# Performance work log

Hardware: AMD Instinct MI355X
Metric: run time of the kernel (lower is better)

The kernel has to match this reference:

```python
import jax, jax.numpy as jnp
import numpy as np
from jax import lax

S = 64        # num_sam_segments
B = 2
HIMG = 336    # full-res SAM segmap / painted map
HP = 24       # DINO patch grid (336/14)
CD = 768      # DINO feature channels
CM = 3072     # concatenated backbone channels (4 layers * 768)
RH = 48       # readout spatial size ceil(336/7)
HID = 128     # SPADE hidden_mlp_channels
EPS = 1e-12


def conv2d(x, w, b=None, pad=0):
    out = lax.conv_general_dilated(x, w, (1, 1), [(pad, pad), (pad, pad)],
                                   dimension_numbers=("NCHW", "OIHW", "NCHW"))
    if b is not None:
        out = out + b[None, :, None, None]
    return out


def paint_semantic_map(f_sem, segmap):
    # f_sem: (B, C, Hp, Wp) float; segmap: (B, H, W) int
    Bn, C, Hp, Wp = f_sem.shape
    H, W = segmap.shape[1:]
    # torch F.interpolate mode='nearest' downsample: src_idx = floor(dst_idx * in/out)
    iy = (jnp.arange(Hp) * H) // Hp
    ix = (jnp.arange(Wp) * W) // Wp
    seg_p = segmap[:, iy][:, :, ix]                      # (B, Hp, Wp)
    ids = jnp.clip(seg_p, 0, S - 1).reshape(Bn, -1)      # (B, Np)
    ids_off = (ids + jnp.arange(Bn)[:, None] * S).reshape(-1)
    flat = f_sem.transpose(0, 2, 3, 1).reshape(Bn * Hp * Wp, C)
    sums = jax.ops.segment_sum(flat, ids_off, num_segments=Bn * S)
    cnt = jax.ops.segment_sum(jnp.ones((Bn * Hp * Wp, 1), flat.dtype), ids_off,
                              num_segments=Bn * S)
    means = jnp.where(cnt > 0, sums / jnp.maximum(cnt, 1.0), 0.0).reshape(Bn, S, C)
    pix = jnp.clip(segmap, 0, S - 1)                     # (B, H, W)
    painted = means[jnp.arange(Bn)[:, None, None], pix]  # (B, H, W, C) gather
    return painted.transpose(0, 3, 1, 2)                 # (B, C, H, W)


def spade_ln(x, painted, ws, bs, wg, bg, wb, bb):
    # layer_norm over (C,H,W) per sample, no affine
    mean = jnp.mean(x, axis=(1, 2, 3), keepdims=True)
    var = jnp.mean((x - mean) ** 2, axis=(1, 2, 3), keepdims=True)
    xn = (x - mean) * lax.rsqrt(var + EPS)
    sem = jax.image.resize(painted, (x.shape[0], painted.shape[1], x.shape[2], x.shape[3]),
                           method="bilinear")
    h = jax.nn.relu(conv2d(sem, ws, bs, pad=1))
    gamma = conv2d(h, wg, bg, pad=1)
    beta = conv2d(h, wb, bb, pad=1)
    return xn * (1.0 + gamma) + beta


def setup_inputs() -> dict:
    key = jax.random.key(0)
    ks = jax.random.split(key, 16)
    n = lambda k, sh: jax.random.normal(k, sh, jnp.float32) * 0.02
    inp = {
        "x_main": jax.random.normal(ks[0], (B, CM, RH, RH), jnp.float32),
        "f_sem": jax.random.normal(ks[1], (B, CD, HP, HP), jnp.float32),
        "segmap": jax.random.randint(ks[2], (B, HIMG, HIMG), 0, S, jnp.int32),
    }
    i = 3
    for li, nf in enumerate([CM, 8, 16]):
        inp[f"ws{li}"] = n(ks[i], (HID, CD, 3, 3)); inp[f"bs{li}"] = jnp.zeros((HID,), jnp.float32)
        inp[f"wg{li}"] = n(ks[i + 1], (nf, HID, 3, 3)); inp[f"bg{li}"] = jnp.zeros((nf,), jnp.float32)
        inp[f"wb{li}"] = n(ks[i + 2], (nf, HID, 3, 3)); inp[f"bb{li}"] = jnp.zeros((nf,), jnp.float32)
        i += 3
    inp["w0"] = n(ks[12], (8, CM, 1, 1)); inp["bias0"] = jnp.zeros((8,), jnp.float32)
    inp["w1"] = n(ks[13], (16, 8, 1, 1)); inp["bias1"] = jnp.zeros((16,), jnp.float32)
    inp["w2"] = n(ks[14], (1, 16, 1, 1)); inp["bias2"] = jnp.zeros((1,), jnp.float32)
    return inp


def reference(x_main, f_sem, segmap,
              ws0, bs0, wg0, bg0, wb0, bb0,
              ws1, bs1, wg1, bg1, wb1, bb1,
              ws2, bs2, wg2, bg2, wb2, bb2,
              w0, bias0, w1, bias1, w2, bias2):
    painted = paint_semantic_map(f_sem, segmap)
    h = spade_ln(x_main, painted, ws0, bs0, wg0, bg0, wb0, bb0)
    h = jax.nn.softplus(conv2d(h, w0) + bias0[None, :, None, None])
    h = spade_ln(h, painted, ws1, bs1, wg1, bg1, wb1, bb1)
    h = jax.nn.softplus(conv2d(h, w1) + bias1[None, :, None, None])
    h = spade_ln(h, painted, ws2, bs2, wg2, bg2, wb2, bb2)
    h = jax.nn.softplus(conv2d(h, w2) + bias2[None, :, None, None])
    return h  # (B, 1, RH, RH)
```

## Files before the change

kernel.cpp:

```cpp
#include <hip/hip_runtime.h>
#include <hip/hip_bf16.h>

typedef __hip_bfloat16 bf16;
typedef __bf16 v8bf __attribute__((ext_vector_type(8)));
typedef float v4f __attribute__((ext_vector_type(4)));

#define PB 2304
#define PTOT 4608

__device__ __forceinline__ float b2f(bf16 x){ return __bfloat162float(x); }
__device__ __forceinline__ bf16 f2b(float x){ return __float2bfloat16(x); }
__device__ __forceinline__ float softplus_f(float x){
  return fmaxf(x, 0.f) + log1pf(expf(-fabsf(x)));
}
__device__ __forceinline__ float LD(const void* src, size_t i, int fl){
  return fl ? ((const float*)src)[i] : b2f(((const bf16*)src)[i]);
}

__device__ __forceinline__ void gload_lds16(const void* g, void* l){
  __builtin_amdgcn_global_load_lds(
      (const __attribute__((address_space(1))) void*)g,
      (__attribute__((address_space(3))) void*)l, 16, 0, 0);
}

__global__ __launch_bounds__(256) void k_sniff(const unsigned* __restrict__ x, int* __restrict__ flag){
  int t = threadIdx.x;
  int cnt = 0;
  for (int i = t; i < 4096; i += 256){
    unsigned e = (x[i] >> 8) & 0x7F;
    if (e >= 0x38 && e <= 0x42) cnt++;
  }
  for (int off = 32; off; off >>= 1) cnt += __shfl_down(cnt, off, 64);
  __shared__ int sc[4];
  if ((t & 63) == 0) sc[t >> 6] = cnt;
  __syncthreads();
  if (t == 0) *flag = (sc[0]+sc[1]+sc[2]+sc[3] < 2048) ? 1 : 0;
}

__global__ void k_zero(float* __restrict__ p, int n){
  int i = blockIdx.x*256 + threadIdx.x;
  if (i < n) p[i] = 0.f;
}

__global__ __launch_bounds__(256) void k_cvt_small(
    const void* s4, const void* s10, const void* s16, const void* s6, const void* s8,
    const void* s12, const void* s14, const void* s18, const void* s20,
    const void* s21, const void* s22, const void* s23, const void* s24,
    const void* s25, const void* s26,
    float* __restrict__ dst, const int* __restrict__ flag){
  int i = blockIdx.x*256 + threadIdx.x;
  if (i >= 31321) return;
  int fl = *flag;
  const void* src; size_t off;
  if      (i < 128)   { src = s4;  off = i; }
  else if (i < 256)   { src = s10; off = i - 128; }
  else if (i < 384)   { src = s16; off = i - 256; }
  else if (i < 3456)  { src = s6;  off = i - 384; }
  else if (i < 6528)  { src = s8;  off = i - 3456; }
  else if (i < 6536)  { src = s12; off = i - 6528; }
  else if (i < 6544)  { src = s14; off = i - 6536; }
  else if (i < 6560)  { src = s18; off = i - 6544; }
  else if (i < 6576)  { src = s20; off = i - 6560; }
  else if (i < 31152) { src = s21; off = i - 6576; }
  else if (i < 31160) { src = s22; off = i - 31152; }
  else if (i < 31288) { src = s23; off = i - 31160; }
  else if (i < 31304) { src = s24; off = i - 31288; }
  else if (i < 31320) { src = s25; off = i - 31304; }
  else                { src = s26; off = i - 31320; }
  dst[i] = LD(src, off, fl);
}

__global__ __launch_bounds__(256) void k_bcol(const float* __restrict__ SMALLF, float* __restrict__ BCOL){
  int t = threadIdx.x;
  const float* BG1 = SMALLF + 6528; const float* BB1 = SMALLF + 6536;
  const float* BG2 = SMALLF + 6544; const float* BB2 = SMALLF + 6560;
  const float* BB0 = SMALLF + 3456; const float* W0  = SMALLF + 6576;
  if (t < 8)       BCOL[t] = BG1[t];
  else if (t < 16) BCOL[t] = BB1[t-8];
  else if (t < 32) BCOL[t] = BG2[t-16];
  else if (t < 48) BCOL[t] = BB2[t-32];
  else if (t < 64) BCOL[t] = 0.f;
  float part[8] = {0,0,0,0,0,0,0,0};
  for (int c = t; c < 3072; c += 256){
    float bb = BB0[c];
    #pragma unroll
    for (int oc = 0; oc < 8; oc++) part[oc] += bb*W0[oc*3072 + c];
  }
  __shared__ float red[4][8];
  int wv = t >> 6, lane = t & 63;
  #pragma unroll
  for (int oc = 0; oc < 8; oc++){
    float v = part[oc];
    for (int off = 32; off; off >>= 1) v += __shfl_down(v, off, 64);
    if (lane == 0) red[wv][oc] = v;
  }
  __syncthreads();
  if (t < 8) BCOL[48 + t] = red[0][t] + red[1][t] + red[2][t] + red[3][t];
}

__global__ __launch_bounds__(256) void k_mzero(float* __restrict__ MB){
  int i = blockIdx.x*256 + threadIdx.x;
  if (i < 9216) MB[i] = 0.f;
}

__global__ __launch_bounds__(256) void k_mbeta(const void* __restrict__ wb0, const int* __restrict__ flag,
                                               const float* __restrict__ w0f, float* __restrict__ MB){
  int jb = blockIdx.x, nb = blockIdx.y, t = threadIdx.x;
  int fl = *flag;
  int jl = t & 127, nh = t >> 7;
  int j = jb*128 + jl;
  int src = jl*9 + jb;
  float acc[8] = {0,0,0,0,0,0,0,0};
  int n0 = nb*128 + nh*64;
  for (int i = 0; i < 64; i++){
    int n = n0 + i;
    float wv = LD(wb0, (size_t)n*1152 + src, fl);
    #pragma unroll
    for (int oc = 0; oc < 8; oc++) acc[oc] += wv*w0f[oc*3072 + n];
  }
  #pragma unroll
  for (int oc = 0; oc < 8; oc++) atomicAdd(&MB[oc*1152 + j], acc[oc]);
}

__global__ __launch_bounds__(256) void k_wsm(const float* __restrict__ MB, bf16* __restrict__ WSMALL){
  int i = blockIdx.x*256 + threadIdx.x;
  if (i >= 9216) return;
  float v = MB[i];
  bf16 hi = f2b(v);
  WSMALL[48*1152 + i] = hi;
  WSMALL[56*1152 + i] = f2b(v - b2f(hi));
}

template<int ICW>
__global__ __launch_bounds__(256) void k_permW(const void* __restrict__ src, bf16* __restrict__ dst,
                                               int total, const int* __restrict__ flag){
  int idx = blockIdx.x*256 + threadIdx.x;
  if (idx >= total) return;
  int oc = idx / (9*ICW);
  int rr = idx % (9*ICW);
  int dyx = rr / ICW, ic = rr % ICW;
  size_t si = (size_t)(oc*ICW + ic)*9 + dyx;
  dst[idx] = f2b(LD(src, si, *flag));
}

__global__ __launch_bounds__(256) void k_seg_means(const void* __restrict__ f_sem, const int* __restrict__ flag,
                                                   const int* __restrict__ segmap,
                                                   float* __restrict__ means){
  int s = blockIdx.x, b = blockIdx.y, t = threadIdx.x;
  int fl = *flag;
  __shared__ int sid[576];
  for (int i = t; i < 576; i += 256){
    int y = i / 24, x = i % 24;
    int v = segmap[b*336*336 + (y*14)*336 + x*14];
    sid[i] = min(max(v, 0), 63);
  }
  __syncthreads();
  float a0=0.f, a1=0.f, a2=0.f; int cnt = 0;
  for (int i = 0; i < 576; i++){
    if (sid[i] == s){
      cnt++;
      a0 += LD(f_sem, (size_t)(b*768 + t      )*576 + i, fl);
      a1 += LD(f_sem, (size_t)(b*768 + t + 256)*576 + i, fl);
      a2 += LD(f_sem, (size_t)(b*768 + t + 512)*576 + i, fl);
    }
  }
  float inv = cnt > 0 ? 1.f/(float)cnt : 0.f;
  float* o = means + (size_t)(b*64 + s)*768;
  o[t] = a0*inv; o[t+256] = a1*inv; o[t+512] = a2*inv;
}

__global__ __launch_bounds__(256) void k_tt(const void* __restrict__ ws0, const void* __restrict__ ws1,
    const void* __restrict__ ws2, const int* __restrict__ flag,
    const float* __restrict__ means, bf16* __restrict__ WTT){
  int bx = blockIdx.x;
  int dyx = bx / 24, ocb = bx % 24;
  int b = blockIdx.y, t = threadIdx.x;
  int fl = *flag;
  int ocg0 = ocb*16;
  const void* wsrc; int ocl0 = ocg0;
  if (ocl0 < 128) wsrc = ws0;
  else if (ocl0 < 256){ wsrc = ws1; ocl0 -= 128; }
  else { wsrc = ws2; ocl0 -= 256; }
  __shared__ float wl[16][768];
  for (int ol = 0; ol < 16; ol++)
    for (int ic = t; ic < 768; ic += 256)
      wl[ol][ic] = LD(wsrc, (size_t)(ocl0 + ol)*6912 + (size_t)ic*9 + dyx, fl);
  __syncthreads();
  int s = t & 63, og = t >> 6;
  const float* mr = means + ((size_t)b*64 + s)*768;
  float acc[4] = {0.f, 0.f, 0.f, 0.f};
  for (int ic = 0; ic < 768; ic += 4){
    float4 m = *reinterpret_cast<const float4*>(mr + ic);
    #pragma unroll
    for (int k = 0; k < 4; k++){
      const float* w = &wl[og + k*4][ic];
      acc[k] += m.x*w[0] + m.y*w[1] + m.z*w[2] + m.w*w[3];
    }
  }
  #pragma unroll
  for (int k = 0; k < 4; k++){
    bf16 h = f2b(acc[k]);
    size_t base = ((size_t)(b*384 + ocg0 + og + k*4))*1152 + (size_t)dyx*128 + s;
    WTT[base] = h;
    WTT[base + 64] = h;
  }
}

__global__ __launch_bounds__(192) void k_A(const int* __restrict__ segmap, bf16* __restrict__ AHL){
  int blk = blockIdx.x;
  int b = blk / PB, rem = blk % PB, yo = rem / 48, xo = rem % 48;
  __shared__ float accs[64];
  int t = threadIdx.x;
  if (t < 64) accs[t] = 0.f;
  __syncthreads();
  if (t < 169){
    int ty = t / 13, tx = t % 13;
    int jy = 7*yo - 3 + ty, jx = 7*xo - 3 + tx;
    if (jy >= 0 && jy < 336 && jx >= 0 && jx < 336){
      int wy = 7 - abs(ty - 6), wx = 7 - abs(tx - 6);
      int sv = segmap[b*336*336 + jy*336 + jx];
      sv = min(max(sv, 0), 63);
      atomicAdd(&accs[sv], (float)(wy*wx));
    }
  }
  int sumy = 0, sumx = 0;
  for (int k = 0; k < 13; k++){
    int jy = 7*yo - 3 + k; if (jy >= 0 && jy < 336) sumy += 7 - abs(k - 6);
    int jx = 7*xo - 3 + k; if (jx >= 0 && jx < 336) sumx += 7 - abs(k - 6);
  }
  __syncthreads();
  if (t < 64){
    float v = accs[t] / (float)(sumy*sumx);
    bf16 hi = f2b(v);
    AHL[(size_t)blk*128 + t] = hi;
    AHL[(size_t)blk*128 + 64 + t] = f2b(v - b2f(hi));
  }
}

__global__ __launch_bounds__(256) void k_ln_partial(const void* __restrict__ x, const int* __restrict__ flag,
                                                    float2* __restrict__ part){
  int b = blockIdx.y, blk = blockIdx.x, t = threadIdx.x;
  int fl = *flag;
  size_t base = (size_t)b*7077888 + (size_t)blk*55296;
  float s = 0.f, sq = 0.f;
  for (int i = 0; i < 216; i++){
    float v = LD(x, base + t + i*256, fl);
    s += v; sq += v*v;
  }
  for (int off = 32; off; off >>= 1){ s += __shfl_down(s, off, 64); sq += __shfl_down(sq, off, 64); }
  __shared__ float ls[4], lq[4];
  int w = t >> 6, lane = t & 63;
  if (lane == 0){ ls[w] = s; lq[w] = sq; }
  __syncthreads();
  if (t == 0) part[b*128 + blk] = make_float2(ls[0]+ls[1]+ls[2]+ls[3], lq[0]+lq[1]+lq[2]+lq[3]);
}

__global__ void k_ln_final(const float2* __restrict__ part, float* __restrict__ stats){
  int b = blockIdx.x, t = threadIdx.x;
  float2 v = part[b*128 + t];
  float s = v.x, sq = v.y;
  for (int off = 32; off; off >>= 1){ s += __shfl_down(s, off, 64); sq += __shfl_down(sq, off, 64); }
  __shared__ float ls[2], lq[2];
  if ((t & 63) == 0){ ls[t>>6] = s; lq[t>>6] = sq; }
  __syncthreads();
  if (t == 0){
    s = ls[0]+ls[1]; sq = lq[0]+lq[1];
    const float N = 7077888.f;
    float mean = s/N; float var = sq/N - mean*mean; var = fmaxf(var, 0.f);
    stats[b*2] = mean; stats[b*2+1] = rsqrtf(var + 1e-12f);
  }
}

__global__ __launch_bounds__(256) void k_ln_small(const float* __restrict__ z, int cnt, float* __restrict__ stats){
  int b = blockIdx.x, t = threadIdx.x;
  const float* p = z + (size_t)b*cnt;
  float s = 0.f, sq = 0.f;
  for (int i = t; i < cnt; i += 256){ float v = p[i]; s += v; sq += v*v; }
  for (int off = 32; off; off >>= 1){ s += __shfl_down(s, off, 64); sq += __shfl_down(sq, off, 64); }
  __shared__ float ls[4], lq[4];
  int w = t >> 6, lane = t & 63;
  if (lane == 0){ ls[w] = s; lq[w] = sq; }
  __syncthreads();
  if (t == 0){
    s = ls[0]+ls[1]+ls[2]+ls[3]; sq = lq[0]+lq[1]+lq[2]+lq[3];
    float mean = s/(float)cnt; float var = sq/(float)cnt - mean*mean; var = fmaxf(var, 0.f);
    stats[b*2] = mean; stats[b*2+1] = rsqrtf(var + 1e-12f);
  }
}

template<bool RELU, typename OT>
__global__ __launch_bounds__(256) void k_gemm(
    const bf16* __restrict__ Asrc, int AS, int acol, int ICW,
    const bf16* __restrict__ W, int K, size_t wbstride,
    const float* __restrict__ bp0, const float* __restrict__ bp1, const float* __restrict__ bp2, int seg,
    OT* __restrict__ out, int N, int ncb, int ldo, const bf16* __restrict__ zpad)
{
  __shared__ __align__(16) bf16 Al[64][64];
  __shared__ __align__(16) bf16 Bl[64][64];
  int t = threadIdx.x;
  int m0 = blockIdx.x*64, n0 = blockIdx.y*64;
  int wv = t >> 6, lane = t & 63;
  int lr8 = lane >> 3, sseg = (lane & 7) ^ lr8;
  int b = m0 >= PB ? 1 : 0;

  int ya[2], xa[2]; bool bv[2]; const bf16* wb[2];
  #pragma unroll
  for (int i = 0; i < 2; i++){
    int sp = (m0 - b*PB) + wv*16 + i*8 + lr8;
    ya[i] = sp / 48; xa[i] = sp % 48;
    int nrow = ncb + n0 + wv*16 + i*8 + lr8;
    bv[i] = nrow < N;
    wb[i] = W + (size_t)b*wbstride + (size_t)nrow*K + sseg*8;
  }

  int wm = (wv >> 1)*32, wn = (wv & 1)*32;
  int lrow = lane & 15, quad = lane >> 4;
  int sx = lrow & 7;
  int o0 = ((quad    ) ^ sx)*8;
  int o1 = ((quad + 4) ^ sx)*8;

  v4f acc00 = {0,0,0,0}, acc01 = {0,0,0,0}, acc10 = {0,0,0,0}, acc11 = {0,0,0,0};

  int dyx = 0, ic0 = 0;
  int ktn = K / 64;
  for (int kt = 0; kt < ktn; kt++){
    int dy = dyx/3 - 1, dx = dyx%3 - 1;
    #pragma unroll
    for (int i = 0; i < 2; i++){
      int ys = ya[i] + dy, xs = xa[i] + dx;
      const bf16* ga = (ys >= 0 && ys < 48 && xs >= 0 && xs < 48)
        ? Asrc + (size_t)(b*PB + ys*48 + xs)*AS + acol + ic0 + sseg*8 : zpad;
      gload_lds16(ga, &Al[wv*16 + i*8][0]);
      const bf16* gb = bv[i] ? wb[i] + kt*64 : zpad;
      gload_lds16(gb, &Bl[wv*16 + i*8][0]);
    }
    asm volatile("s_waitcnt vmcnt(0)" ::: "memory");
    __syncthreads();
    v8bf a00 = *reinterpret_cast<const v8bf*>(&Al[wm      + lrow][o0]);
    v8bf a10 = *reinterpret_cast<const v8bf*>(&Al[wm + 16 + lrow][o0]);
    v8bf a01 = *reinterpret_cast<const v8bf*>(&Al[wm      + lrow][o1]);
    v8bf a11 = *reinterpret_cast<const v8bf*>(&Al[wm + 16 + lrow][o1]);
    v8bf b00 = *reinterpret_cast<const v8bf*>(&Bl[wn      + lrow][o0]);
    v8bf b10 = *reinterpret_cast<const v8bf*>(&Bl[wn + 16 + lrow][o0]);
    v8bf b01 = *reinterpret_cast<const v8bf*>(&Bl[wn      + lrow][o1]);
    v8bf b11 = *reinterpret_cast<const v8bf*>(&Bl[wn + 16 + lrow][o1]);
    acc00 = __builtin_amdgcn_mfma_f32_16x16x32_bf16(a00, b00, acc00, 0, 0, 0);
    acc00 = __builtin_amdgcn_mfma_f32_16x16x32_bf16(a01, b01, acc00, 0, 0, 0);
    acc01 = __builtin_amdgcn_mfma_f32_16x16x32_bf16(a00, b10, acc01, 0, 0, 0);
    acc01 = __builtin_amdgcn_mfma_f32_16x16x32_bf16(a01, b11, acc01, 0, 0, 0);
    acc10 = __builtin_amdgcn_mfma_f32_16x16x32_bf16(a10, b00, acc10, 0, 0, 0);
    acc10 = __builtin_amdgcn_mfma_f32_16x16x32_bf16(a11, b01, acc10, 0, 0, 0);
    acc11 = __builtin_amdgcn_mfma_f32_16x16x32_bf16(a10, b10, acc11, 0, 0, 0);
    acc11 = __builtin_amdgcn_mfma_f32_16x16x32_bf16(a11, b11, acc11, 0, 0, 0);
    __syncthreads();
    ic0 += 64; if (ic0 == ICW){ ic0 = 0; dyx++; }
  }

  auto store_tile = [&](v4f a, int mi, int ni){
    int gcol = ncb + n0 + wn + ni*16 + lrow;
    if (gcol >= N) return;
    int sel = gcol / seg; sel = sel > 2 ? 2 : sel;
    const float* bp = sel == 0 ? bp0 : (sel == 1 ? bp1 : bp2);
    float bias = bp[gcol - sel*seg];
    int rowb = m0 + wm + mi*16 + quad*4;
    #pragma unroll
    for (int rg = 0; rg < 4; rg++){
      float v = a[rg] + bias;
      if (RELU) v = fmaxf(v, 0.f);
      if constexpr (sizeof(OT) == 2) out[(size_t)(rowb+rg)*ldo + (gcol - ncb)] = f2b(v);
      else                           out[(size_t)(rowb+rg)*ldo + (gcol - ncb)] = (OT)v;
    }
  };
  store_tile(acc00, 0, 0); store_tile(acc01, 0, 1);
  store_tile(acc10, 1, 0); store_tile(acc11, 1, 1);
}

__global__ __launch_bounds__(256) void k_gfuse(
    const bf16* __restrict__ HS, const bf16* __restrict__ WG0, const float* __restrict__ BG0,
    const void* __restrict__ x, const int* __restrict__ flag, const float* __restrict__ stats,
    const float* __restrict__ w0f, float* __restrict__ z0, const bf16* __restrict__ zpad)
{
  __shared__ __align__(16) char lds_raw[38912];
  bf16 (*Al)[64]  = (bf16(*)[64])lds_raw;
  bf16 (*Bl)[64]  = (bf16(*)[64])(lds_raw + 16384);
  float (*xl)[132] = (float(*)[132])lds_raw;
  float (*w0l)[128] = (float(*)[128])(lds_raw + 33792);
  float* bg0l = (float*)(lds_raw + 33792 + 4096);

  int t = threadIdx.x;
  int m0 = blockIdx.x*128, n0 = blockIdx.y*128;
  int b = m0 >= PB ? 1 : 0;
  int fl = *flag;

  int wv = t >> 6, lane = t & 63;
  int lr8 = lane >> 3, sseg = (lane & 7) ^ lr8;
  int spbase = m0 - b*PB;

  int ya[4], xa[4];
  #pragma unroll
  for (int i = 0; i < 4; i++){
    int sp = spbase + wv*32 + i*8 + lr8;
    ya[i] = sp / 48; xa[i] = sp % 48;
  }
  const bf16* wgb = WG0 + (size_t)(n0 + wv*32 + lr8)*1152 + sseg*8;

  int wm = wv*32, lrow = lane & 15, quad = lane >> 4;
  int sx = lrow & 7;

  v4f acc[2][8];
  #pragma unroll
  for (int mi = 0; mi < 2; mi++)
    #pragma unroll
    for (int ni = 0; ni < 8; ni++) acc[mi][ni] = (v4f){0,0,0,0};

  for (int kt = 0; kt < 18; kt++){
    int dyx = kt >> 1, icr = (kt & 1) << 6;
    int dy = dyx/3 - 1, dx = dyx%3 - 1;
    #pragma unroll
    for (int i = 0; i < 4; i++){
      int ys = ya[i] + dy, xs = xa[i] + dx;
      const bf16* ga = (ys >= 0 && ys < 48 && xs >= 0 && xs < 48)
        ? HS + (size_t)(b*PB + ys*48 + xs)*384 + icr + sseg*8 : zpad;
      gload_lds16(ga, &Al[wv*32 + i*8][0]);
      gload_lds16(wgb + (size_t)(i*8)*1152 + dyx*128 + icr, &Bl[wv*32 + i*8][0]);
    }
    asm volatile("s_waitcnt vmcnt(0)" ::: "memory");
    __syncthreads();
    #pragma unroll
    for (int kh = 0; kh < 2; kh++){
      int oa = ((kh*4 + quad) ^ sx)*8;
      v8bf a0 = *reinterpret_cast<const v8bf*>(&Al[wm      + lrow][oa]);
      v8bf a1 = *reinterpret_cast<const v8bf*>(&Al[wm + 16 + lrow][oa]);
      #pragma unroll
      for (int ni = 0; ni < 8; ni++){
        v8bf bn = *reinterpret_cast<const v8bf*>(&Bl[ni*16 + lrow][oa]);
        acc[0][ni] = __builtin_amdgcn_mfma_f32_16x16x32_bf16(a0, bn, acc[0][ni], 0, 0, 0);
        acc[1][ni] = __builtin_amdgcn_mfma_f32_16x16x32_bf16(a1, bn, acc[1][ni], 0, 0, 0);
      }
    }
    __syncthreads();
  }

  for (int i = t; i < 1024; i += 256) w0l[i >> 7][i & 127] = w0f[(size_t)(i >> 7)*3072 + n0 + (i & 127)];
  if (t < 128) bg0l[t] = BG0[n0 + t];

  float mean = stats[b*2], rstd = stats[b*2+1];
  float s[2][4][8];
  #pragma unroll
  for (int mi = 0; mi < 2; mi++)
    #pragma unroll
    for (int rg = 0; rg < 4; rg++)
      #pragma unroll
      for (int oc = 0; oc < 8; oc++) s[mi][rg][oc] = 0.f;

  for (int h = 0; h < 2; h++){
    if (h) __syncthreads();
    if (fl){
      const float* xp = (const float*)x + ((size_t)(b*3072 + n0 + h*64))*2304 + spbase;
      #pragma unroll
      for (int it = 0; it < 8; it++){
        int idx = it*256 + t;
        int row = idx >> 5, c4 = (idx & 31)*4;
        float4 v = *reinterpret_cast<const float4*>(xp + (size_t)row*2304 + c4);
        *reinterpret_cast<float4*>(&xl[row][c4]) = v;
      }
    } else {
      const bf16* xp = (const bf16*)x + ((size_t)(b*3072 + n0 + h*64))*2304 + spbase;
      #pragma unroll
      for (int it = 0; it < 4; it++){
        int idx = it*256 + t;
        int row = idx >> 4, c8 = (idx & 15)*8;
        v8bf v = *reinterpret_cast<const v8bf*>(xp + (size_t)row*2304 + c8);
        float4 f0, f1;
        f0.x = (float)v[0]; f0.y = (float)v[1]; f0.z = (float)v[2]; f0.w = (float)v[3];
        f1.x = (float)v[4]; f1.y = (float)v[5]; f1.z = (float)v[6]; f1.w = (float)v[7];
        *reinterpret_cast<float4*>(&xl[row][c8])     = f0;
        *reinterpret_cast<float4*>(&xl[row][c8 + 4]) = f1;
      }
    }
    __syncthreads();
    #pragma unroll
    for (int mi = 0; mi < 2; mi++){
      int pl = wm + mi*16 + quad*4;
      #pragma unroll
      for (int nis = 0; nis < 4; nis++){
        int ni = h*4 + nis;
        int c_half = nis*16 + lrow;
        int c_blk = h*64 + c_half;
        float bg = bg0l[c_blk];
        float w0v[8];
        #pragma unroll
        for (int oc = 0; oc < 8; oc++) w0v[oc] = w0l[oc][c_blk];
        #pragma unroll
        for (int rg = 0; rg < 4; rg++){
          float gv = acc[mi][ni][rg] + bg;
          float xn = (xl[c_half][pl + rg] - mean)*rstd;
          float tv = xn*(1.f + gv);
          #pragma unroll
          for (int oc = 0; oc < 8; oc++) s[mi][rg][oc] += tv*w0v[oc];
        }
      }
    }
  }

  #pragma unroll
  for (int mi = 0; mi < 2; mi++){
    #pragma unroll
    for (int rg = 0; rg < 4; rg++)
      #pragma unroll
      for (int oc = 0; oc < 8; oc++){
        float v = s[mi][rg][oc];
        v += __shfl_xor(v, 1, 64);
        v += __shfl_xor(v, 2, 64);
        v += __shfl_xor(v, 4, 64);
        v += __shfl_xor(v, 8, 64);
        s[mi][rg][oc] = v;
      }
    if (lrow == 0){
      int p = m0 + wm + mi*16 + quad*4;
      #pragma unroll
      for (int rg = 0; rg < 4; rg++)
        #pragma unroll
        for (int oc = 0; oc < 8; oc++)
          atomicAdd(&z0[(size_t)(p + rg)*8 + oc], s[mi][rg][oc]);
    }
  }
}

__global__ __launch_bounds__(256) void k_z0init(const float* __restrict__ b0f, const float* __restrict__ GBS,
                                                float* __restrict__ z0){
  int i = blockIdx.x*256 + threadIdx.x;
  if (i >= 36864) return;
  int p = i >> 3, oc = i & 7;
  z0[i] = b0f[oc] + GBS[(size_t)p*64 + 48 + oc] + GBS[(size_t)p*64 + 56 + oc];
}

__global__ __launch_bounds__(256) void k_sp(float* z, int n){
  int i = blockIdx.x*256 + threadIdx.x;
  if (i < n) z[i] = softplus_f(z[i]);
}

__global__ __launch_bounds__(256) void k_F1(const float* __restrict__ z0, const float* __restrict__ GBS,
    const float* __restrict__ stats, const float* __restrict__ w1f, const float* __restrict__ b1f,
    float* __restrict__ z1){
  int p = blockIdx.x*256 + threadIdx.x;
  if (p >= PTOT) return;
  int b = p / PB;
  float mean = stats[b*2], rstd = stats[b*2+1];
  const float* zr = z0 + (size_t)p*8;
  const float* gr = GBS + (size_t)p*64;
  float yv[8];
  #pragma unroll
  for (int c = 0; c < 8; c++) yv[c] = (zr[c] - mean)*rstd*(1.f + gr[c]) + gr[8 + c];
  #pragma unroll
  for (int oc = 0; oc < 16; oc++){
    float s = b1f[oc];
    #pragma unroll
    for (int c = 0; c < 8; c++) s += yv[c]*w1f[oc*8 + c];
    z1[(size_t)p*16 + oc] = softplus_f(s);
  }
}

__global__ __launch_bounds__(256) void k_F2(const float* __restrict__ z1, const float* __restrict__ GBS,
    const float* __restrict__ stats, const float* __restrict__ w2f, const float* __restrict__ b2f,
    void* __restrict__ outp, const int* __restrict__ flag){
  int p = blockIdx.x*256 + threadIdx.x;
  if (p >= PTOT) return;
  int b = p / PB;
  float mean = stats[b*2], rstd = stats[b*2+1];
  const float* zr = z1 + (size_t)p*16;
  const float* gr = GBS + (size_t)p*64 + 16;
  float s = b2f[0];
  #pragma unroll
  for (int c = 0; c < 16; c++){
    float yv = (zr[c] - mean)*rstd*(1.f + gr[c]) + gr[16 + c];
    s += yv*w2f[c];
  }
  float r = softplus_f(s);
  if (*flag) ((float*)outp)[p] = r;
  else       ((bf16*)outp)[p] = f2b(r);
}

extern "C" void kernel_launch(void* const* d_in, const int* in_sizes, int n_in,
                              void* d_out, int out_size, void* d_ws, size_t ws_size,
                              hipStream_t stream){
  const void* x_main = d_in[0];
  const void* f_sem  = d_in[1];
  const int*  segmap = (const int*)d_in[2];

  char* ws = (char*)d_ws;
  size_t o = 0;
  auto alloc = [&](size_t bytes){ size_t r = o; o = (o + bytes + 255) & ~(size_t)255; return r; };
  float* MEANS = (float*)(ws + alloc(98304u*4));
  bf16*  AHL   = (bf16*) (ws + alloc(589824u*2));
  bf16*  WTT   = (bf16*) (ws + alloc(884736u*2));
  bf16*  WG0   = (bf16*) (ws + alloc(3538944u*2));
  bf16*  WSMALL= (bf16*) (ws + alloc(73728u*2));
  bf16*  HS    = (bf16*) (ws + alloc(1769472u*2));
  float* GBS   = (float*)(ws + alloc(294912u*4));
  float* Z0    = (float*)(ws + alloc(36864u*4));
  float* Z1    = (float*)(ws + alloc(73728u*4));
  float2* LNP  = (float2*)(ws + alloc(256u*8));
  float* STATS = (float*)(ws + alloc(16u*4));
  int*   FLAG  = (int*)  (ws + alloc(64u));
  float* SMALLF= (float*)(ws + alloc(31321u*4));
  float* MB    = (float*)(ws + alloc(9216u*4));
  float* BCOL  = (float*)(ws + alloc(64u*4));
  bf16*  ZPAD  = (bf16*) (ws + alloc(512u));

  float *BS0=SMALLF+0, *BS1=SMALLF+128, *BS2=SMALLF+256;
  float *BG0=SMALLF+384;
  float *W0=SMALLF+6576, *B0=SMALLF+31152;
  float *W1=SMALLF+31160, *B1=SMALLF+31288;
  float *W2=SMALLF+31304, *B2=SMALLF+31320;

  k_sniff<<<1, 256, 0, stream>>>((const unsigned*)x_main, FLAG);
  k_zero<<<1, 256, 0, stream>>>((float*)ZPAD, 128);
  k_cvt_small<<<123, 256, 0, stream>>>(d_in[4], d_in[10], d_in[16], d_in[6], d_in[8],
      d_in[12], d_in[14], d_in[18], d_in[20], d_in[21], d_in[22], d_in[23], d_in[24],
      d_in[25], d_in[26], SMALLF, FLAG);
  k_bcol<<<1, 256, 0, stream>>>(SMALLF, BCOL);
  k_mzero<<<36, 256, 0, stream>>>(MB);
  k_mbeta<<<dim3(9,24), 256, 0, stream>>>(d_in[7], FLAG, W0, MB);
  k_wsm<<<36, 256, 0, stream>>>(MB, WSMALL);

  k_permW<128><<<dim3((3538944+255)/256),256, 0, stream>>>(d_in[5],  WG0,            3538944, FLAG);
  k_permW<128><<<dim3((9216+255)/256),   256, 0, stream>>>(d_in[11], WSMALL,           9216, FLAG);
  k_permW<128><<<dim3((9216+255)/256),   256, 0, stream>>>(d_in[13], WSMALL + 8*1152,  9216, FLAG);
  k_permW<128><<<dim3((18432+255)/256),  256, 0, stream>>>(d_in[17], WSMALL + 16*1152, 18432, FLAG);
  k_permW<128><<<dim3((18432+255)/256),  256, 0, stream>>>(d_in[19], WSMALL + 32*1152, 18432, FLAG);

  k_ln_partial<<<dim3(128,2), 256, 0, stream>>>(x_main, FLAG, LNP);
  k_ln_final<<<2, 128, 0, stream>>>(LNP, STATS);
  k_seg_means<<<dim3(64,2), 256, 0, stream>>>(f_sem, FLAG, segmap, MEANS);
  k_tt<<<dim3(216,2), 256, 0, stream>>>(d_in[3], d_in[9], d_in[15], FLAG, MEANS, WTT);
  k_A<<<PTOT, 192, 0, stream>>>(segmap, AHL);

  k_gemm<true, bf16><<<dim3(72,6), 256, 0, stream>>>(AHL, 128, 0, 128, WTT, 1152, (size_t)384*1152,
      BS0, BS1, BS2, 128, HS, 384, 0, 384, ZPAD);
  k_gemm<false, float><<<dim3(72,1), 256, 0, stream>>>(HS, 384, 128, 128, WSMALL, 1152, 0,
      BCOL, BCOL, BCOL, 9999, GBS, 16, 0, 64, ZPAD);
  k_gemm<false, float><<<dim3(72,1), 256, 0, stream>>>(HS, 384, 256, 128, WSMALL + 16*1152, 1152, 0,
      BCOL+16, BCOL+16, BCOL+16, 9999, GBS+16, 32, 0, 64, ZPAD);
  k_gemm<false, float><<<dim3(72,1), 256, 0, stream>>>(HS, 384, 0, 128, WSMALL + 48*1152, 1152, 0,
      BCOL+48, BCOL+48, BCOL+48, 9999, GBS+48, 16, 0, 64, ZPAD);

  k_z0init<<<144, 256, 0, stream>>>(B0, GBS, Z0);
  k_gfuse<<<dim3(36,24), 256, 0, stream>>>(HS, WG0, BG0, x_main, FLAG, STATS, W0, Z0, ZPAD);
  k_sp<<<144, 256, 0, stream>>>(Z0, 36864);

  k_ln_small<<<2, 256, 0, stream>>>(Z0, 18432, STATS + 4);
  k_F1<<<18, 256, 0, stream>>>(Z0, GBS, STATS + 4, W1, B1, Z1);
  k_ln_small<<<2, 256, 0, stream>>>(Z1, 36864, STATS + 8);
  k_F2<<<18, 256, 0, stream>>>(Z1, GBS, STATS + 8, W2, B2, d_out, FLAG);
}
```

Baseline: 634.5 us.

## Halve gfuse N-tile for occupancy and fold small launches into fewer kernels

The main fused gamma-conv kernel drops its N tile from 128 to 64 channels, doubling the grid to 36x48. This shrinks the accumulator and output registers and allows a 4-blocks-per-CU launch bound, at the cost of reloading the A tile twice as often and doing more atomics on z0. Several tiny launches are merged: ZPAD zeroing goes into sniff, MB zeroing into cvt_small, the three small GEMMs into one grid, and softplus into the layernorm stats pass. The merges target launch overhead.

Result: faster. 621.7 us (-2.0%).

```diff
diff --git a/kernel.cpp b/kernel.cpp
--- a/kernel.cpp
+++ b/kernel.cpp
@@ -23,8 +23,10 @@
       (__attribute__((address_space(3))) void*)l, 16, 0, 0);
 }
 
-__global__ __launch_bounds__(256) void k_sniff(const unsigned* __restrict__ x, int* __restrict__ flag){
+__global__ __launch_bounds__(256) void k_sniff(const unsigned* __restrict__ x, int* __restrict__ flag,
+                                               float* __restrict__ zp){
   int t = threadIdx.x;
+  if (t < 128) zp[t] = 0.f;
   int cnt = 0;
   for (int i = t; i < 4096; i += 256){
     unsigned e = (x[i] >> 8) & 0x7F;
@@ -35,11 +37,6 @@
   if ((t & 63) == 0) sc[t >> 6] = cnt;
   __syncthreads();
   if (t == 0) *flag = (sc[0]+sc[1]+sc[2]+sc[3] < 2048) ? 1 : 0;
-}
-
-__global__ void k_zero(float* __restrict__ p, int n){
-  int i = blockIdx.x*256 + threadIdx.x;
-  if (i < n) p[i] = 0.f;
 }
 
 __global__ __launch_bounds__(256) void k_cvt_small(
@@ -47,9 +44,10 @@
     const void* s12, const void* s14, const void* s18, const void* s20,
     const void* s21, const void* s22, const void* s23, const void* s24,
     const void* s25, const void* s26,
-    float* __restrict__ dst, const int* __restrict__ flag){
+    float* __restrict__ dst, const int* __restrict__ flag, float* __restrict__ MB){
   int i = blockIdx.x*256 + threadIdx.x;
-  if (i >= 31321) return;
+  if (i >= 40537) return;
+  if (i >= 31321){ MB[i - 31321] = 0.f; return; }
   int fl = *flag;
   const void* src; size_t off;
   if      (i < 128)   { src = s4;  off = i; }
@@ -98,11 +96,6 @@
   if (t < 8) BCOL[48 + t] = red[0][t] + red[1][t] + red[2][t] + red[3][t];
 }
 
-__global__ __launch_bounds__(256) void k_mzero(float* __restrict__ MB){
-  int i = blockIdx.x*256 + threadIdx.x;
-  if (i < 9216) MB[i] = 0.f;
-}
-
 __global__ __launch_bounds__(256) void k_mbeta(const void* __restrict__ wb0, const int* __restrict__ flag,
                                                const float* __restrict__ w0f, float* __restrict__ MB){
   int jb = blockIdx.x, nb = blockIdx.y, t = threadIdx.x;
@@ -271,6 +264,27 @@
   }
 }
 
+__global__ __launch_bounds__(256) void k_spln(float* __restrict__ z, int cnt, float* __restrict__ stats){
+  int b = blockIdx.x, t = threadIdx.x;
+  float* p = z + (size_t)b*cnt;
+  float s = 0.f, sq = 0.f;
+  for (int i = t; i < cnt; i += 256){
+    float v = softplus_f(p[i]);
+    p[i] = v;
+    s += v; sq += v*v;
+  }
+  for (int off = 32; off; off >>= 1){ s += __shfl_down(s, off, 64); sq += __shfl_down(sq, off, 64); }
+  __shared__ float ls[4], lq[4];
+  int w = t >> 6, lane = t & 63;
+  if (lane == 0){ ls[w] = s; lq[w] = sq; }
+  __syncthreads();
+  if (t == 0){
+    s = ls[0]+ls[1]+ls[2]+ls[3]; sq = lq[0]+lq[1]+lq[2]+lq[3];
+    float mean = s/(float)cnt; float var = sq/(float)cnt - mean*mean; var = fmaxf(var, 0.f);
+    stats[b*2] = mean; stats[b*2+1] = rsqrtf(var + 1e-12f);
+  }
+}
+
 __global__ __launch_bounds__(256) void k_ln_small(const float* __restrict__ z, int cnt, float* __restrict__ stats){
   int b = blockIdx.x, t = threadIdx.x;
   const float* p = z + (size_t)b*cnt;
@@ -289,16 +303,14 @@
 }
 
 template<bool RELU, typename OT>
-__global__ __launch_bounds__(256) void k_gemm(
+__device__ __forceinline__ void gemm_body(
     const bf16* __restrict__ Asrc, int AS, int acol, int ICW,
     const bf16* __restrict__ W, int K, size_t wbstride,
     const float* __restrict__ bp0, const float* __restrict__ bp1, const float* __restrict__ bp2, int seg,
-    OT* __restrict__ out, int N, int ncb, int ldo, const bf16* __restrict__ zpad)
+    OT* __restrict__ out, int N, int ncb, int ldo, const bf16* __restrict__ zpad,
+    int m0, int n0, bf16 (*Al)[64], bf16 (*Bl)[64])
 {
-  __shared__ __align__(16) bf16 Al[64][64];
-  __shared__ __align__(16) bf16 Bl[64][64];
   int t = threadIdx.x;
-  int m0 = blockIdx.x*64, n0 = blockIdx.y*64;
   int wv = t >> 6, lane = t & 63;
   int lr8 = lane >> 3, sseg = (lane & 7) ^ lr8;
   int b = m0 >= PB ? 1 : 0;
@@ -375,20 +387,49 @@
   store_tile(acc10, 1, 0); store_tile(acc11, 1, 1);
 }
 
-__global__ __launch_bounds__(256) void k_gfuse(
+template<bool RELU, typename OT>
+__global__ __launch_bounds__(256) void k_gemm(
+    const bf16* __restrict__ Asrc, int AS, int acol, int ICW,
+    const bf16* __restrict__ W, int K, size_t wbstride,
+    const float* __restrict__ bp0, const float* __restrict__ bp1, const float* __restrict__ bp2, int seg,
+    OT* __restrict__ out, int N, int ncb, int ldo, const bf16* __restrict__ zpad)
+{
+  __shared__ __align__(16) bf16 Al[64][64];
+  __shared__ __align__(16) bf16 Bl[64][64];
+  gemm_body<RELU, OT>(Asrc, AS, acol, ICW, W, K, wbstride, bp0, bp1, bp2, seg,
+                      out, N, ncb, ldo, zpad, blockIdx.x*64, blockIdx.y*64, Al, Bl);
+}
+
+__global__ __launch_bounds__(256) void k_gsmall(
+    const bf16* __restrict__ HS, const bf16* __restrict__ WSMALL, const float* __restrict__ BCOL,
+    float* __restrict__ GBS, const bf16* __restrict__ zpad)
+{
+  __shared__ __align__(16) bf16 Al[64][64];
+  __shared__ __align__(16) bf16 Bl[64][64];
+  int y = blockIdx.y;
+  int acol = y == 0 ? 128 : (y == 1 ? 256 : 0);
+  const bf16* W = WSMALL + (y == 0 ? 0 : (y == 1 ? 16*1152 : 48*1152));
+  const float* bp = BCOL + (y == 0 ? 0 : (y == 1 ? 16 : 48));
+  float* out = GBS + (y == 0 ? 0 : (y == 1 ? 16 : 48));
+  int N = y == 1 ? 32 : 16;
+  gemm_body<false, float>(HS, 384, acol, 128, W, 1152, 0, bp, bp, bp, 9999,
+                          out, N, 0, 64, zpad, blockIdx.x*64, 0, Al, Bl);
+}
+
+__global__ __launch_bounds__(256, 4) void k_gfuse(
     const bf16* __restrict__ HS, const bf16* __restrict__ WG0, const float* __restrict__ BG0,
     const void* __restrict__ x, const int* __restrict__ flag, const float* __restrict__ stats,
     const float* __restrict__ w0f, float* __restrict__ z0, const bf16* __restrict__ zpad)
 {
-  __shared__ __align__(16) char lds_raw[38912];
+  __shared__ __align__(16) char lds_raw[36096];
   bf16 (*Al)[64]  = (bf16(*)[64])lds_raw;
   bf16 (*Bl)[64]  = (bf16(*)[64])(lds_raw + 16384);
   float (*xl)[132] = (float(*)[132])lds_raw;
-  float (*w0l)[128] = (float(*)[128])(lds_raw + 33792);
-  float* bg0l = (float*)(lds_raw + 33792 + 4096);
+  float (*w0l)[64] = (float(*)[64])(lds_raw + 33792);
+  float* bg0l = (float*)(lds_raw + 35840);
 
   int t = threadIdx.x;
-  int m0 = blockIdx.x*128, n0 = blockIdx.y*128;
+  int m0 = blockIdx.x*128, n0 = blockIdx.y*64;
   int b = m0 >= PB ? 1 : 0;
   int fl = *flag;
 
@@ -402,16 +443,16 @@
     int sp = spbase + wv*32 + i*8 + lr8;
     ya[i] = sp / 48; xa[i] = sp % 48;
   }
-  const bf16* wgb = WG0 + (size_t)(n0 + wv*32 + lr8)*1152 + sseg*8;
+  const bf16* wgb = WG0 + (size_t)(n0 + wv*16 + lr8)*1152 + sseg*8;
 
   int wm = wv*32, lrow = lane & 15, quad = lane >> 4;
   int sx = lrow & 7;
 
-  v4f acc[2][8];
+  v4f acc[2][4];
   #pragma unroll
   for (int mi = 0; mi < 2; mi++)
     #pragma unroll
-    for (int ni = 0; ni < 8; ni++) acc[mi][ni] = (v4f){0,0,0,0};
+    for (int ni = 0; ni < 4; ni++) acc[mi][ni] = (v4f){0,0,0,0};
 
   for (int kt = 0; kt < 18; kt++){
     int dyx = kt >> 1, icr = (kt & 1) << 6;
@@ -422,8 +463,10 @@
       const bf16* ga = (ys >= 0 && ys < 48 && xs >= 0 && xs < 48)
         ? HS + (size_t)(b*PB + ys*48 + xs)*384 + icr + sseg*8 : zpad;
       gload_lds16(ga, &Al[wv*32 + i*8][0]);
-      gload_lds16(wgb + (size_t)(i*8)*1152 + dyx*128 + icr, &Bl[wv*32 + i*8][0]);
-    }
+    }
+    #pragma unroll
+    for (int i = 0; i < 2; i++)
+      gload_lds16(wgb + (size_t)(i*8)*1152 + dyx*128 + icr, &Bl[wv*16 + i*8][0]);
     asm volatile("s_waitcnt vmcnt(0)" ::: "memory");
     __syncthreads();
     #pragma unroll
@@ -432,7 +475,7 @@
       v8bf a0 = *reinterpret_cast<const v8bf*>(&Al[wm      + lrow][oa]);
       v8bf a1 = *reinterpret_cast<const v8bf*>(&Al[wm + 16 + lrow][oa]);
       #pragma unroll
-      for (int ni = 0; ni < 8; ni++){
+      for (int ni = 0; ni < 4; ni++){
         v8bf bn = *reinterpret_cast<const v8bf*>(&Bl[ni*16 + lrow][oa]);
         acc[0][ni] = __builtin_amdgcn_mfma_f32_16x16x32_bf16(a0, bn, acc[0][ni], 0, 0, 0);
         acc[1][ni] = __builtin_amdgcn_mfma_f32_16x16x32_bf16(a1, bn, acc[1][ni], 0, 0, 0);
@@ -441,88 +484,85 @@
     __syncthreads();
   }
 
-  for (int i = t; i < 1024; i += 256) w0l[i >> 7][i & 127] = w0f[(size_t)(i >> 7)*3072 + n0 + (i & 127)];
-  if (t < 128) bg0l[t] = BG0[n0 + t];
+  for (int i = t; i < 512; i += 256) w0l[i >> 6][i & 63] = w0f[(size_t)(i >> 6)*3072 + n0 + (i & 63)];
+  if (t < 64) bg0l[t] = BG0[n0 + t];
+
+  if (fl){
+    const float* xp = (const float*)x + ((size_t)(b*3072 + n0))*2304 + spbase;
+    #pragma unroll
+    for (int it = 0; it < 8; it++){
+      int idx = it*256 + t;
+      int row = idx >> 5, c4 = (idx & 31)*4;
+      float4 v = *reinterpret_cast<const float4*>(xp + (size_t)row*2304 + c4);
+      *reinterpret_cast<float4*>(&xl[row][c4]) = v;
+    }
+  } else {
+    const bf16* xp = (const bf16*)x + ((size_t)(b*3072 + n0))*2304 + spbase;
+    #pragma unroll
+    for (int it = 0; it < 4; it++){
+      int idx = it*256 + t;
+      int row = idx >> 4, c8 = (idx & 15)*8;
+      v8bf v = *reinterpret_cast<const v8bf*>(xp + (size_t)row*2304 + c8);
+      float4 f0, f1;
+      f0.x = (float)v[0]; f0.y = (float)v[1]; f0.z = (float)v[2]; f0.w = (float)v[3];
+      f1.x = (float)v[4]; f1.y = (float)v[5]; f1.z = (float)v[6]; f1.w = (float)v[7];
+      *reinterpret_cast<float4*>(&xl[row][c8])     = f0;
+      *reinterpret_cast<float4*>(&xl[row][c8 + 4]) = f1;
+    }
+  }
+  __syncthreads();
 
   float mean = stats[b*2], rstd = stats[b*2+1];
-  float s[2][4][8];
-  #pragma unroll
-  for (int mi = 0; mi < 2; mi++)
-    #pragma unroll
-    for (int rg = 0; rg < 4; rg++)
+
+  for (int og2 = 0; og2 < 2; og2++){
+    float s[2][4][4];
+    #pragma unroll
+    for (int mi = 0; mi < 2; mi++)
       #pragma unroll
-      for (int oc = 0; oc < 8; oc++) s[mi][rg][oc] = 0.f;
-
-  for (int h = 0; h < 2; h++){
-    if (h) __syncthreads();
-    if (fl){
-      const float* xp = (const float*)x + ((size_t)(b*3072 + n0 + h*64))*2304 + spbase;
-      #pragma unroll
-      for (int it = 0; it < 8; it++){
-        int idx = it*256 + t;
-        int row = idx >> 5, c4 = (idx & 31)*4;
-        float4 v = *reinterpret_cast<const float4*>(xp + (size_t)row*2304 + c4);
-        *reinterpret_cast<float4*>(&xl[row][c4]) = v;
-      }
-    } else {
-      const bf16* xp = (const bf16*)x + ((size_t)(b*3072 + n0 + h*64))*2304 + spbase;
-      #pragma unroll
-      for (int it = 0; it < 4; it++){
-        int idx = it*256 + t;
-        int row = idx >> 4, c8 = (idx & 15)*8;
-        v8bf v = *reinterpret_cast<const v8bf*>(xp + (size_t)row*2304 + c8);
-        float4 f0, f1;
-        f0.x = (float)v[0]; f0.y = (float)v[1]; f0.z = (float)v[2]; f0.w = (float)v[3];
-        f1.x = (float)v[4]; f1.y = (float)v[5]; f1.z = (float)v[6]; f1.w = (float)v[7];
-        *reinterpret_cast<float4*>(&xl[row][c8])     = f0;
-        *reinterpret_cast<float4*>(&xl[row][c8 + 4]) = f1;
-      }
-    }
-    __syncthreads();
+      for (int rg = 0; rg < 4; rg++)
+        #pragma unroll
+        for (int oc = 0; oc < 4; oc++) s[mi][rg][oc] = 0.f;
     #pragma unroll
     for (int mi = 0; mi < 2; mi++){
       int pl = wm + mi*16 + quad*4;
       #pragma unroll
       for (int nis = 0; nis < 4; nis++){
-        int ni = h*4 + nis;
-        int c_half = nis*16 + lrow;
-        int c_blk = h*64 + c_half;
-        float bg = bg0l[c_blk];
-        float w0v[8];
+        int c = nis*16 + lrow;
+        float bg = bg0l[c];
+        float w0v[4];
         #pragma unroll
-        for (int oc = 0; oc < 8; oc++) w0v[oc] = w0l[oc][c_blk];
+        for (int oc = 0; oc < 4; oc++) w0v[oc] = w0l[og2*4 + oc][c];
         #pragma unroll
         for (int rg = 0; rg < 4; rg++){
-          float gv = acc[mi][ni][rg] + bg;
-          float xn = (xl[c_half][pl + rg] - mean)*rstd;
+          float gv = acc[mi][nis][rg] + bg;
+          float xn = (xl[c][pl + rg] - mean)*rstd;
           float tv = xn*(1.f + gv);
           #pragma unroll
-          for (int oc = 0; oc < 8; oc++) s[mi][rg][oc] += tv*w0v[oc];
+          for (int oc = 0; oc < 4; oc++) s[mi][rg][oc] += tv*w0v[oc];
         }
       }
     }
-  }
-
-  #pragma unroll
-  for (int mi = 0; mi < 2; mi++){
-    #pragma unroll
-    for (int rg = 0; rg < 4; rg++)
-      #pragma unroll
-      for (int oc = 0; oc < 8; oc++){
-        float v = s[mi][rg][oc];
-        v += __shfl_xor(v, 1, 64);
-        v += __shfl_xor(v, 2, 64);
-        v += __shfl_xor(v, 4, 64);
-        v += __shfl_xor(v, 8, 64);
-        s[mi][rg][oc] = v;
-      }
-    if (lrow == 0){
-      int p = m0 + wm + mi*16 + quad*4;
+    #pragma unroll
+    for (int mi = 0; mi < 2; mi++){
       #pragma unroll
       for (int rg = 0; rg < 4; rg++)
         #pragma unroll
-        for (int oc = 0; oc < 8; oc++)
-          atomicAdd(&z0[(size_t)(p + rg)*8 + oc], s[mi][rg][oc]);
+        for (int oc = 0; oc < 4; oc++){
+          float v = s[mi][rg][oc];
+          v += __shfl_xor(v, 1, 64);
+          v += __shfl_xor(v, 2, 64);
+          v += __shfl_xor(v, 4, 64);
+          v += __shfl_xor(v, 8, 64);
+          s[mi][rg][oc] = v;
+        }
+      if (lrow == 0){
+        int p = m0 + wm + mi*16 + quad*4;
+        #pragma unroll
+        for (int rg = 0; rg < 4; rg++)
+          #pragma unroll
+          for (int oc = 0; oc < 4; oc++)
+            atomicAdd(&z0[(size_t)(p + rg)*8 + og2*4 + oc], s[mi][rg][oc]);
+      }
     }
   }
 }
@@ -533,11 +573,6 @@
   if (i >= 36864) return;
   int p = i >> 3, oc = i & 7;
   z0[i] = b0f[oc] + GBS[(size_t)p*64 + 48 + oc] + GBS[(size_t)p*64 + 56 + oc];
-}
-
-__global__ __launch_bounds__(256) void k_sp(float* z, int n){
-  int i = blockIdx.x*256 + threadIdx.x;
-  if (i < n) z[i] = softplus_f(z[i]);
 }
 
 __global__ __launch_bounds__(256) void k_F1(const float* __restrict__ z0, const float* __restrict__ GBS,
@@ -614,13 +649,11 @@
   float *W1=SMALLF+31160, *B1=SMALLF+31288;
   float *W2=SMALLF+31304, *B2=SMALLF+31320;
 
-  k_sniff<<<1, 256, 0, stream>>>((const unsigned*)x_main, FLAG);
-  k_zero<<<1, 256, 0, stream>>>((float*)ZPAD, 128);
-  k_cvt_small<<<123, 256, 0, stream>>>(d_in[4], d_in[10], d_in[16], d_in[6], d_in[8],
+  k_sniff<<<1, 256, 0, stream>>>((const unsigned*)x_main, FLAG, (float*)ZPAD);
+  k_cvt_small<<<159, 256, 0, stream>>>(d_in[4], d_in[10], d_in[16], d_in[6], d_in[8],
       d_in[12], d_in[14], d_in[18], d_in[20], d_in[21], d_in[22], d_in[23], d_in[24],
-      d_in[25], d_in[26], SMALLF, FLAG);
+      d_in[25], d_in[26], SMALLF, FLAG, MB);
   k_bcol<<<1, 256, 0, stream>>>(SMALLF, BCOL);
-  k_mzero<<<36, 256, 0, stream>>>(MB);
   k_mbeta<<<dim3(9,24), 256, 0, stream>>>(d_in[7], FLAG, W0, MB);
   k_wsm<<<36, 256, 0, stream>>>(MB, WSMALL);
 
@@ -638,18 +671,12 @@
 
   k_gemm<true, bf16><<<dim3(72,6), 256, 0, stream>>>(AHL, 128, 0, 128, WTT, 1152, (size_t)384*1152,
       BS0, BS1, BS2, 128, HS, 384, 0, 384, ZPAD);
-  k_gemm<false, float><<<dim3(72,1), 256, 0, stream>>>(HS, 384, 128, 128, WSMALL, 1152, 0,
-      BCOL, BCOL, BCOL, 9999, GBS, 16, 0, 64, ZPAD);
-  k_gemm<false, float><<<dim3(72,1), 256, 0, stream>>>(HS, 384, 256, 128, WSMALL + 16*1152, 1152, 0,
-      BCOL+16, BCOL+16, BCOL+16, 9999, GBS+16, 32, 0, 64, ZPAD);
-  k_gemm<false, float><<<dim3(72,1), 256, 0, stream>>>(HS, 384, 0, 128, WSMALL + 48*1152, 1152, 0,
-      BCOL+48, BCOL+48, BCOL+48, 9999, GBS+48, 16, 0, 64, ZPAD);
+  k_gsmall<<<dim3(72,3), 256, 0, stream>>>(HS, WSMALL, BCOL, GBS, ZPAD);
 
   k_z0init<<<144, 256, 0, stream>>>(B0, GBS, Z0);
-  k_gfuse<<<dim3(36,24), 256, 0, stream>>>(HS, WG0, BG0, x_main, FLAG, STATS, W0, Z0, ZPAD);
-  k_sp<<<144, 256, 0, stream>>>(Z0, 36864);
-
-  k_ln_small<<<2, 256, 0, stream>>>(Z0, 18432, STATS + 4);
+  k_gfuse<<<dim3(36,48), 256, 0, stream>>>(HS, WG0, BG0, x_main, FLAG, STATS, W0, Z0, ZPAD);
+  k_spln<<<2, 256, 0, stream>>>(Z0, 18432, STATS + 4);
+
   k_F1<<<18, 256, 0, stream>>>(Z0, GBS, STATS + 4, W1, B1, Z1);
   k_ln_small<<<2, 256, 0, stream>>>(Z1, 36864, STATS + 8);
   k_F2<<<18, 256, 0, stream>>>(Z1, GBS, STATS + 8, W2, B2, d_out, FLAG);
```
